# Performance work log

Measured on AMD Instinct MI355X. Metric: run time of the kernel, lower is better.

The kernel has to match this reference:

```python
import jax, jax.numpy as jnp
import numpy as np

M, K, N = 8192, 4096, 4096  # tokens, in_features, out_features


def setup_inputs() -> dict:
    key = jax.random.key(0)
    k1, k2, k3, k4 = jax.random.split(key, 4)
    inp = jax.random.normal(k1, (M, K), dtype=jnp.float32)
    # int8-range weights stored as int32 host-side; [out_features, in_features] like torch Linear
    weight = jax.random.randint(k2, (N, K), -128, 128, dtype=jnp.int32)
    weight_scale = jax.random.uniform(k3, (N,), dtype=jnp.float32, minval=1e-3, maxval=2e-2)
    bias = jax.random.normal(k4, (N,), dtype=jnp.float32)
    return {"input": inp, "weight": weight, "weight_scale": weight_scale, "bias": bias}


def reference(input, weight, weight_scale, bias):
    # --- init-time transforms (W8A8IntLinear.__init__) ---
    wq = weight.T.astype(jnp.int8)                                   # [K, N]
    azp_adj = jnp.sum(wq.astype(jnp.int32), axis=0, keepdims=True)    # [1, N] int32 column sums

    # --- dynamic asymmetric per-token int8 quantization (scaled_int8_quant) ---
    x_max = jnp.max(input, axis=-1, keepdims=True)                    # [M, 1]
    x_min = jnp.min(input, axis=-1, keepdims=True)                    # [M, 1]
    scale = (x_max - x_min) / 255.0                                   # per-token scale
    azp = jnp.round(-128.0 - x_min / scale).astype(jnp.int32)         # per-token zero point
    q = jnp.clip(jnp.round(input / scale).astype(jnp.int32) + azp, -128, 127).astype(jnp.int8)

    # --- int8 GEMM with int32 accumulation (cutlass_scaled_mm_azp) ---
    acc = jnp.matmul(q, wq, preferred_element_type=jnp.int32)         # [M, N] int32
    corrected = (acc - azp * azp_adj).astype(jnp.float32)             # zero-point correction
    return scale * weight_scale[None, :] * corrected + bias[None, :]
```

## Files before the change

### kernel.cpp

```cpp
#include <hip/hip_runtime.h>
#include <cstdint>
#include <cstddef>


#define M_DIM 8192
#define K_DIM 4096
#define N_DIM 4096

typedef int v4i __attribute__((ext_vector_type(4)));

__global__ __launch_bounds__(256) void quant_kernel(
    const float* __restrict__ x, signed char* __restrict__ q,
    float* __restrict__ scale_out, int* __restrict__ azp_out)
{
    const int m = blockIdx.x;
    const int t = threadIdx.x;
    const float4* row4 = (const float4*)(x + (size_t)m * K_DIM);

    float4 v[4];
    float mx = -3.4e38f, mn = 3.4e38f;
#pragma unroll
    for (int i = 0; i < 4; ++i) {
        v[i] = row4[i * 256 + t];
        mx = fmaxf(mx, fmaxf(fmaxf(v[i].x, v[i].y), fmaxf(v[i].z, v[i].w)));
        mn = fminf(mn, fminf(fminf(v[i].x, v[i].y), fminf(v[i].z, v[i].w)));
    }
#pragma unroll
    for (int off = 32; off; off >>= 1) {
        mx = fmaxf(mx, __shfl_down(mx, off));
        mn = fminf(mn, __shfl_down(mn, off));
    }
    __shared__ float smx[4], smn[4];
    if ((t & 63) == 0) { smx[t >> 6] = mx; smn[t >> 6] = mn; }
    __syncthreads();
    mx = fmaxf(fmaxf(smx[0], smx[1]), fmaxf(smx[2], smx[3]));
    mn = fminf(fminf(smn[0], smn[1]), fminf(smn[2], smn[3]));

    const float scale = (mx - mn) / 255.0f;
    const int azp = (int)rintf(-128.0f - mn / scale);
    if (t == 0) { scale_out[m] = scale; azp_out[m] = azp; }

    int* qrow = (int*)(q + (size_t)m * K_DIM);
    const float* vf = (const float*)v;
#pragma unroll
    for (int i = 0; i < 4; ++i) {
        int b[4];
#pragma unroll
        for (int j = 0; j < 4; ++j) {
            int qv = (int)rintf(vf[4 * i + j] / scale) + azp;
            qv = qv < -128 ? -128 : (qv > 127 ? 127 : qv);
            b[j] = qv;
        }
        qrow[i * 256 + t] =
            (b[0] & 255) | ((b[1] & 255) << 8) | ((b[2] & 255) << 16) | ((b[3] & 255) << 24);
    }
}

__global__ __launch_bounds__(256) void wprep_kernel(
    const int* __restrict__ w, signed char* __restrict__ w8, int* __restrict__ azp_adj)
{
    const int n = blockIdx.x;
    const int t = threadIdx.x;
    const int4* row = (const int4*)(w + (size_t)n * K_DIM);
    int* w8row = (int*)(w8 + (size_t)n * K_DIM);
    int sum = 0;
#pragma unroll
    for (int i = 0; i < 4; ++i) {
        int4 a = row[i * 256 + t];
        sum += a.x + a.y + a.z + a.w;
        w8row[i * 256 + t] =
            (a.x & 255) | ((a.y & 255) << 8) | ((a.z & 255) << 16) | ((a.w & 255) << 24);
    }
#pragma unroll
    for (int off = 32; off; off >>= 1) sum += __shfl_down(sum, off);
    __shared__ int ssum[4];
    if ((t & 63) == 0) ssum[t >> 6] = sum;
    __syncthreads();
    if (t == 0) azp_adj[n] = ssum[0] + ssum[1] + ssum[2] + ssum[3];
}

__device__ __forceinline__ void async_copy16(const signed char* g, signed char* l) {
    __builtin_amdgcn_global_load_lds(
        (const __attribute__((address_space(1))) void*)g,
        (__attribute__((address_space(3))) void*)l, 16, 0, 0);
}

__global__ __launch_bounds__(256) void gemm_kernel(
    const signed char* __restrict__ A,
    const signed char* __restrict__ B,
    const float* __restrict__ scale, const int* __restrict__ azp,
    const int* __restrict__ azp_adj, const float* __restrict__ wscale,
    const float* __restrict__ bias, float* __restrict__ out)
{
    __shared__ signed char sA[128 * 64];
    __shared__ signed char sB[128 * 64];

    const int t = threadIdx.x;
    const int wave = t >> 6;
    const int lane = t & 63;
    const int quad = lane >> 4;
    const int r16 = lane & 15;

    const int bm = blockIdx.y * 128;
    const int bn = blockIdx.x * 128;
    const int wm = (wave >> 1) * 64;
    const int wn = (wave & 1) * 64;

    v4i acc[4][4];
#pragma unroll
    for (int i = 0; i < 4; ++i)
#pragma unroll
        for (int j = 0; j < 4; ++j) acc[i][j] = (v4i){0, 0, 0, 0};

    const int srow = t >> 2;
    const int scol = ((t & 3) ^ ((t >> 3) & 3)) * 16;
    const signed char* ag0 = A + (size_t)(bm + srow) * K_DIM + scol;
    const signed char* ag1 = A + (size_t)(bm + 64 + srow) * K_DIM + scol;
    const signed char* bg0 = B + (size_t)(bn + srow) * K_DIM + scol;
    const signed char* bg1 = B + (size_t)(bn + 64 + srow) * K_DIM + scol;

    const v4i* sA4 = (const v4i*)sA;
    const v4i* sB4 = (const v4i*)sB;

    for (int k0 = 0; k0 < K_DIM; k0 += 64) {
        async_copy16(ag0 + k0, sA + t * 16);
        async_copy16(ag1 + k0, sA + 4096 + t * 16);
        async_copy16(bg0 + k0, sB + t * 16);
        async_copy16(bg1 + k0, sB + 4096 + t * 16);
        __syncthreads();

        v4i af[4], bf[4];
#pragma unroll
        for (int i = 0; i < 4; ++i) {
            const int ra = wm + i * 16 + r16;
            const int rb = wn + i * 16 + r16;
            af[i] = sA4[ra * 4 + (quad ^ ((ra >> 1) & 3))];
            bf[i] = sB4[rb * 4 + (quad ^ ((rb >> 1) & 3))];
        }
#pragma unroll
        for (int i = 0; i < 4; ++i)
#pragma unroll
            for (int j = 0; j < 4; ++j)
                acc[i][j] = __builtin_amdgcn_mfma_i32_16x16x64_i8(af[i], bf[j], acc[i][j], 0, 0, 0);
        __syncthreads();
    }

#pragma unroll
    for (int i = 0; i < 4; ++i) {
        const int mbase = bm + wm + i * 16 + quad * 4;
        float sm[4]; int am[4];
#pragma unroll
        for (int r = 0; r < 4; ++r) { sm[r] = scale[mbase + r]; am[r] = azp[mbase + r]; }
#pragma unroll
        for (int j = 0; j < 4; ++j) {
            const int n = bn + wn + j * 16 + r16;
            const float wsn = wscale[n];
            const int adjn = azp_adj[n];
            const float bn_ = bias[n];
#pragma unroll
            for (int r = 0; r < 4; ++r) {
                const int c = acc[i][j][r] - am[r] * adjn;
                out[(size_t)(mbase + r) * N_DIM + n] = sm[r] * wsn * (float)c + bn_;
            }
        }
    }
}

extern "C" void kernel_launch(void* const* d_in, const int* in_sizes, int n_in,
                              void* d_out, int out_size, void* d_ws, size_t ws_size,
                              hipStream_t stream) {
    const float* x      = (const float*)d_in[0];
    const int*   w      = (const int*)d_in[1];
    const float* wscale = (const float*)d_in[2];
    const float* bias   = (const float*)d_in[3];
    float* out = (float*)d_out;

    char* ws = (char*)d_ws;
    signed char* q8  = (signed char*)ws;
    signed char* w8  = (signed char*)(ws + 33554432);
    float* scl       = (float*)(ws + 50331648);
    int*   azp       = (int*)(ws + 50331648 + 32768);
    int*   adj       = (int*)(ws + 50331648 + 65536);

    quant_kernel<<<M_DIM, 256, 0, stream>>>(x, q8, scl, azp);
    wprep_kernel<<<N_DIM, 256, 0, stream>>>(w, w8, adj);
    dim3 grid(N_DIM / 128, M_DIM / 128);
    gemm_kernel<<<grid, 256, 0, stream>>>(q8, w8, scl, azp, adj, wscale, bias, out);
}
```

Baseline: 434.7 us.

## Double-buffer LDS tiles in int8 GEMM to overlap loads with MFMA

Splits the shared-memory A and B tiles into two buffers. The next K-slice is now issued with async global-to-LDS copies while MFMAs run on the current slice, and the two __syncthreads per iteration become a single waitcnt-plus-barrier. This is meant to hide global memory latency behind compute. In exchange LDS use per block doubles to 32KB, which may reduce occupancy. Correctness rests on the single barrier also protecting the buffer being overwritten next.

```diff
diff --git a/kernel.cpp b/kernel.cpp
--- a/kernel.cpp
+++ b/kernel.cpp
@@ -92,8 +92,8 @@
     const int* __restrict__ azp_adj, const float* __restrict__ wscale,
     const float* __restrict__ bias, float* __restrict__ out)
 {
-    __shared__ signed char sA[128 * 64];
-    __shared__ signed char sB[128 * 64];
+    __shared__ signed char sA[2][128 * 64];
+    __shared__ signed char sB[2][128 * 64];
 
     const int t = threadIdx.x;
     const int wave = t >> 6;
@@ -119,30 +119,41 @@
     const signed char* bg0 = B + (size_t)(bn + srow) * K_DIM + scol;
     const signed char* bg1 = B + (size_t)(bn + 64 + srow) * K_DIM + scol;
 
-    const v4i* sA4 = (const v4i*)sA;
-    const v4i* sB4 = (const v4i*)sB;
-
-    for (int k0 = 0; k0 < K_DIM; k0 += 64) {
-        async_copy16(ag0 + k0, sA + t * 16);
-        async_copy16(ag1 + k0, sA + 4096 + t * 16);
-        async_copy16(bg0 + k0, sB + t * 16);
-        async_copy16(bg1 + k0, sB + 4096 + t * 16);
-        __syncthreads();
-
+    async_copy16(ag0, sA[0] + t * 16);
+    async_copy16(ag1, sA[0] + 4096 + t * 16);
+    async_copy16(bg0, sB[0] + t * 16);
+    async_copy16(bg1, sB[0] + 4096 + t * 16);
+
+#pragma unroll 2
+    for (int i = 0; i < 64; ++i) {
+        const int cur = i & 1;
+        const int nxt = cur ^ 1;
+
+        asm volatile("s_waitcnt vmcnt(0)\n\ts_barrier" ::: "memory");
+
+        if (i < 63) {
+            const int kn = (i + 1) << 6;
+            async_copy16(ag0 + kn, sA[nxt] + t * 16);
+            async_copy16(ag1 + kn, sA[nxt] + 4096 + t * 16);
+            async_copy16(bg0 + kn, sB[nxt] + t * 16);
+            async_copy16(bg1 + kn, sB[nxt] + 4096 + t * 16);
+        }
+
+        const v4i* sA4 = (const v4i*)sA[cur];
+        const v4i* sB4 = (const v4i*)sB[cur];
         v4i af[4], bf[4];
 #pragma unroll
-        for (int i = 0; i < 4; ++i) {
-            const int ra = wm + i * 16 + r16;
-            const int rb = wn + i * 16 + r16;
-            af[i] = sA4[ra * 4 + (quad ^ ((ra >> 1) & 3))];
-            bf[i] = sB4[rb * 4 + (quad ^ ((rb >> 1) & 3))];
-        }
-#pragma unroll
-        for (int i = 0; i < 4; ++i)
-#pragma unroll
-            for (int j = 0; j < 4; ++j)
-                acc[i][j] = __builtin_amdgcn_mfma_i32_16x16x64_i8(af[i], bf[j], acc[i][j], 0, 0, 0);
-        __syncthreads();
+        for (int j = 0; j < 4; ++j) {
+            const int ra = wm + j * 16 + r16;
+            const int rb = wn + j * 16 + r16;
+            af[j] = sA4[ra * 4 + (quad ^ ((ra >> 1) & 3))];
+            bf[j] = sB4[rb * 4 + (quad ^ ((rb >> 1) & 3))];
+        }
+#pragma unroll
+        for (int ii = 0; ii < 4; ++ii)
+#pragma unroll
+            for (int jj = 0; jj < 4; ++jj)
+                acc[ii][jj] = __builtin_amdgcn_mfma_i32_16x16x64_i8(af[ii], bf[jj], acc[ii][jj], 0, 0, 0);
     }
 
 #pragma unroll
```

New measurement: 459.9 us. +5.8%, slower.
